# Optimization experiments

Measured on AMD Instinct MI355X. Metric: run time of the kernel, lower is better.

## Reference

```python
import jax, jax.numpy as jnp
import numpy as np
from jax import lax

B, N, C = 16, 16384, 256          # batch, points, seed feature dim
P, NS = 256, 16                   # num_proposal, ball-query nsample
RADIUS = 0.3
NUM_CLASS, NUM_HEADING_BIN, NUM_SIZE = 18, 12, 18
OUT_FEAT = 2 + 3 + NUM_HEADING_BIN * 2 + NUM_SIZE * 4 + NUM_CLASS   # 119
PN2_NC = 128
MID_FEAT = (PN2_NC + OUT_FEAT) // 2                                 # 123
EPS = 1e-5

PARAM_NAMES = [f"mlp_{s}{i}" for i in range(3) for s in ("w", "b", "g", "be")] + [
    "c1_w", "c1_b", "bn1_g", "bn1_b", "c2_w", "c2_b", "bn2_g", "bn2_b", "c3_w", "c3_b"]


def setup_inputs():
    key = jax.random.key(0)
    ks = iter(jax.random.split(key, 32))
    def w(shape):
        return jax.random.normal(next(ks), shape, jnp.float32) / np.float32(np.sqrt(shape[0]))
    inp = {
        "pos":      jax.random.normal(next(ks), (B, N, 3), jnp.float32),
        "features": jax.random.normal(next(ks), (B, C, N), jnp.float32),
        "seed_pos": jax.random.normal(next(ks), (B, N, 3), jnp.float32),
    }
    dims = [3 + C, PN2_NC, PN2_NC, PN2_NC]
    for i in range(3):
        inp[f"mlp_w{i}"]  = w((dims[i], dims[i + 1]))
        inp[f"mlp_b{i}"]  = jnp.zeros((dims[i + 1],), jnp.float32)
        inp[f"mlp_g{i}"]  = jnp.ones((dims[i + 1],), jnp.float32)
        inp[f"mlp_be{i}"] = jnp.zeros((dims[i + 1],), jnp.float32)
    inp["c1_w"], inp["c1_b"] = w((PN2_NC, PN2_NC)), jnp.zeros((PN2_NC,), jnp.float32)
    inp["bn1_g"], inp["bn1_b"] = jnp.ones((PN2_NC,), jnp.float32), jnp.zeros((PN2_NC,), jnp.float32)
    inp["c2_w"], inp["c2_b"] = w((PN2_NC, MID_FEAT)), jnp.zeros((MID_FEAT,), jnp.float32)
    inp["bn2_g"], inp["bn2_b"] = jnp.ones((MID_FEAT,), jnp.float32), jnp.zeros((MID_FEAT,), jnp.float32)
    inp["c3_w"], inp["c3_b"] = w((MID_FEAT, OUT_FEAT)), jnp.zeros((OUT_FEAT,), jnp.float32)
    return inp


def _fps(p):
    # iterative furthest point sampling on one cloud p:[N,3] -> [P] int32 (starts at index 0)
    def step(carry, _):
        dists, far = carry
        d = jnp.sum((p - p[far]) ** 2, axis=-1)
        dists = jnp.minimum(dists, d)
        return (dists, jnp.argmax(dists).astype(jnp.int32)), far
    init = (jnp.full((p.shape[0],), 1e10, p.dtype), jnp.array(0, jnp.int32))
    _, idx = lax.scan(step, init, None, length=P)
    return idx


def _ball_query(new_pos, pos):
    # first NS points of pos within RADIUS of each center (CUDA ball_query semantics)
    d2 = jnp.sum((new_pos[:, :, None, :] - pos[:, None, :, :]) ** 2, -1)  # [B,P,N]
    n = pos.shape[1]
    ar = jnp.arange(n, dtype=jnp.int32)
    sortkey = jnp.where(d2 <= RADIUS ** 2, ar, ar + n)
    vals, idx = lax.top_k(-sortkey, NS)        # smallest keys = earliest in-radius indices
    valid = (-vals) < n
    return jnp.where(valid, idx, idx[..., :1])  # pad misses with first hit


def _bn(x, g, b, axes):
    m = jnp.mean(x, axes, keepdims=True)
    v = jnp.var(x, axes, keepdims=True)
    return (x - m) * lax.rsqrt(v + EPS) * g + b


def _forward(pos, features, seed_pos, params):
    idx_p = jax.vmap(_fps)(seed_pos)                              # seed_fps sampling [B,P]
    take = jax.vmap(lambda a, i: a[i])
    new_pos = take(pos, idx_p)                                    # [B,P,3]
    idx = _ball_query(new_pos, pos)                               # [B,P,NS]
    gp = take(pos, idx.reshape(B, -1)).reshape(B, P, NS, 3)
    gf = take(features.transpose(0, 2, 1), idx.reshape(B, -1)).reshape(B, P, NS, C)
    x = jnp.concatenate([gp - new_pos[:, :, None, :], gf], -1)    # [B,P,NS,3+C]
    for i in range(3):                                            # shared MLP (1x1 conv2d + BN + ReLU)
        x = jax.nn.relu(_bn(x @ params[f"mlp_w{i}"] + params[f"mlp_b{i}"],
                            params[f"mlp_g{i}"], params[f"mlp_be{i}"], (0, 1, 2)))
    x = jnp.max(x, axis=2)                                        # max over neighbors -> [B,P,128]
    x = jax.nn.relu(_bn(x @ params["c1_w"] + params["c1_b"], params["bn1_g"], params["bn1_b"], (0, 1)))
    x = jax.nn.relu(_bn(x @ params["c2_w"] + params["c2_b"], params["bn2_g"], params["bn2_b"], (0, 1)))
    x = x @ params["c3_w"] + params["c3_b"]                       # [B,P,OUT_FEAT]
    return x.transpose(0, 2, 1)                                   # [B,OUT_FEAT,P] like torch Conv1d


def reference(pos, features, seed_pos, mlp_w0, mlp_b0, mlp_g0, mlp_be0, mlp_w1, mlp_b1, mlp_g1, mlp_be1, mlp_w2, mlp_b2, mlp_g2, mlp_be2, c1_w, c1_b, bn1_g, bn1_b, c2_w, c2_b, bn2_g, bn2_b, c3_w, c3_b):
    ps = [mlp_w0, mlp_b0, mlp_g0, mlp_be0, mlp_w1, mlp_b1, mlp_g1, mlp_be1,
          mlp_w2, mlp_b2, mlp_g2, mlp_be2, c1_w, c1_b, bn1_g, bn1_b,
          c2_w, c2_b, bn2_g, bn2_b, c3_w, c3_b]
    params = dict(zip(PARAM_NAMES, ps))
    return _forward(pos, features, seed_pos, params)
```

## Files before the change

### kernel.cpp

```cpp
#include <hip/hip_runtime.h>

#define N_PTS 16384
#define BATCH 16
#define NPROP 256
#define NSAMP 16
#define CFEAT 256
#define KIN 259
#define KPAD 264
#define MBIG 65536
#define MSMALL 4096
#define NOUT 119

#define FPS_LIST(M) M(0) M(1) M(2) M(3) M(4) M(5) M(6) M(7) \
  M(8) M(9) M(10) M(11) M(12) M(13) M(14) M(15) \
  M(16) M(17) M(18) M(19) M(20) M(21) M(22) M(23) \
  M(24) M(25) M(26) M(27) M(28) M(29) M(30) M(31)

#define FPS_PIN8(a,b,c,d,e,f,g,h) \
  asm volatile("" : "+v"(a), "+v"(b), "+v"(c), "+v"(d), \
                    "+v"(e), "+v"(f), "+v"(g), "+v"(h));

__global__ __attribute__((amdgpu_flat_work_group_size(512,512), amdgpu_waves_per_eu(2,2)))
void fps_kernel(const float* __restrict__ sp, int* __restrict__ idx_p) {
#pragma clang fp contract(off)
  const int b = blockIdx.x;
  const int t = threadIdx.x;
  const int w = t >> 6;
  const int lane = t & 63;
  const float* base = sp + (size_t)b * N_PTS * 3;

#define FPS_DECL(J) float px##J, py##J, pz##J, dd##J;
  FPS_LIST(FPS_DECL)
#undef FPS_DECL

#define FPS_INIT(J) { const int i = t + J*512; \
    px##J = base[i*3+0]; py##J = base[i*3+1]; pz##J = base[i*3+2]; \
    dd##J = 1e10f; }
  FPS_LIST(FPS_INIT)
#undef FPS_INIT

  FPS_PIN8(px0,px1,px2,px3,px4,px5,px6,px7)
  FPS_PIN8(px8,px9,px10,px11,px12,px13,px14,px15)
  FPS_PIN8(px16,px17,px18,px19,px20,px21,px22,px23)
  FPS_PIN8(px24,px25,px26,px27,px28,px29,px30,px31)
  FPS_PIN8(py0,py1,py2,py3,py4,py5,py6,py7)
  FPS_PIN8(py8,py9,py10,py11,py12,py13,py14,py15)
  FPS_PIN8(py16,py17,py18,py19,py20,py21,py22,py23)
  FPS_PIN8(py24,py25,py26,py27,py28,py29,py30,py31)
  FPS_PIN8(pz0,pz1,pz2,pz3,pz4,pz5,pz6,pz7)
  FPS_PIN8(pz8,pz9,pz10,pz11,pz12,pz13,pz14,pz15)
  FPS_PIN8(pz16,pz17,pz18,pz19,pz20,pz21,pz22,pz23)
  FPS_PIN8(pz24,pz25,pz26,pz27,pz28,pz29,pz30,pz31)

  if (t == 0) idx_p[b*NPROP] = 0;
  float fx = base[0], fy = base[1], fz = base[2];
  __shared__ unsigned long long part[2][8];
  for (int it = 1; it < NPROP; ++it) {
    float mv = -1.0f; int mi = 0;
#define FPS_STEP(J) { \
    float dx = px##J - fx, dy = py##J - fy, dz = pz##J - fz; \
    float d = (dx*dx + dy*dy) + dz*dz; \
    float nd = fminf(dd##J, d); \
    dd##J = nd; \
    if (nd > mv) { mv = nd; mi = t + J*512; } }
    FPS_LIST(FPS_STEP)
#undef FPS_STEP
    unsigned long long key =
      ((unsigned long long)__float_as_uint(mv) << 32) |
      (unsigned long long)(unsigned)(0x7FFFFFFF - mi);
#pragma unroll
    for (int o = 32; o > 0; o >>= 1) {
      unsigned long long ok = __shfl_xor(key, o, 64);
      if (ok > key) key = ok;
    }
    const int buf = it & 1;
    if (lane == 0) part[buf][w] = key;
    __syncthreads();
    unsigned long long k2 = part[buf][0];
#pragma unroll
    for (int q = 1; q < 8; ++q) {
      unsigned long long ok = part[buf][q];
      if (ok > k2) k2 = ok;
    }
    const int far = 0x7FFFFFFF - (int)(unsigned)(k2 & 0xFFFFFFFFull);
    if (t == 0) idx_p[b*NPROP + it] = far;
    const float* fp = base + (size_t)far*3;
    fx = fp[0]; fy = fp[1]; fz = fp[2];
  }
}

__global__ __launch_bounds__(256)
void newpos_kernel(const float* __restrict__ pos, const int* __restrict__ idx_p,
                   float* __restrict__ npos) {
  int g = blockIdx.x*256 + threadIdx.x;
  if (g >= BATCH*NPROP) return;
  int b = g >> 8;
  int ii = idx_p[g];
  const float* pp = pos + ((size_t)b*N_PTS + ii)*3;
  npos[g*3+0] = pp[0]; npos[g*3+1] = pp[1]; npos[g*3+2] = pp[2];
}

__global__ __launch_bounds__(256)
void ballq_kernel(const float* __restrict__ pos, const float* __restrict__ npos,
                  int* __restrict__ idxg) {
#pragma clang fp contract(off)
  __shared__ int res[4][NSAMP];
  const int tid = threadIdx.x;
  const int w = tid >> 6, lane = tid & 63;
  const int cid = blockIdx.x*4 + w;
  const int b = cid >> 8;
  const float R2 = (float)(0.3*0.3);
  if (lane == 0) res[w][0] = 0;
  const float cx = npos[cid*3+0], cy = npos[cid*3+1], cz = npos[cid*3+2];
  const float* pb = pos + (size_t)b*N_PTS*3;
  int cnt = 0;
  const unsigned long long lmask = (1ull << lane) - 1ull;
#pragma unroll 4
  for (int ch = 0; ch < N_PTS/64; ++ch) {
    int i = ch*64 + lane;
    float dx = pb[i*3+0]-cx, dy = pb[i*3+1]-cy, dz = pb[i*3+2]-cz;
    float d2 = (dx*dx + dy*dy) + dz*dz;
    bool pred = d2 <= R2;
    unsigned long long bal = __ballot(pred);
    if (pred) {
      int slot = cnt + (int)__popcll(bal & lmask);
      if (slot < NSAMP) res[w][slot] = i;
    }
    cnt += (int)__popcll(bal);
  }
  __syncthreads();
  if (lane < NSAMP) {
    int v = res[w][lane];
    if (lane >= cnt) v = res[w][0];
    idxg[cid*NSAMP + lane] = v;
  }
}

__global__ __launch_bounds__(256)
void prep_w(const float* __restrict__ w0, const float* __restrict__ c2w,
            const float* __restrict__ c2b, const float* __restrict__ c3w,
            const float* __restrict__ c3b,
            float* __restrict__ Wp0, float* __restrict__ Wp2, float* __restrict__ B2p,
            float* __restrict__ Wp3, float* __restrict__ B3p) {
  int g = blockIdx.x*256 + threadIdx.x;
  const int S0 = KPAD*128, S1 = S0 + 16384, S2 = S1 + 128, S3 = S2 + 16384, S4 = S3 + 128;
  if (g < S0) {
    int k = g >> 7, n = g & 127;
    Wp0[g] = (k < KIN) ? w0[k*128 + n] : 0.f;
  } else if (g < S1) {
    int g2 = g - S0; int k = g2 >> 7, n = g2 & 127;
    Wp2[g2] = (n < 123) ? c2w[k*123 + n] : 0.f;
  } else if (g < S2) {
    int n = g - S1;
    B2p[n] = (n < 123) ? c2b[n] : 0.f;
  } else if (g < S3) {
    int g2 = g - S2; int k = g2 >> 7, n = g2 & 127;
    Wp3[g2] = (k < 123 && n < NOUT) ? c3w[k*NOUT + n] : 0.f;
  } else if (g < S4) {
    int n = g - S3;
    B3p[n] = (n < NOUT) ? c3b[n] : 0.f;
  }
}

__global__ __launch_bounds__(256)
void gemm_l0(const float* __restrict__ pos, const float* __restrict__ npos,
             const float* __restrict__ feat, const int* __restrict__ idxg,
             const float* __restrict__ Wp, const float* __restrict__ bias,
             float* __restrict__ H) {
  __shared__ float As[8][128];
  __shared__ float Ws[8][128];
  __shared__ float pd[3][128];
  __shared__ int ids[128];
  const int tid = threadIdx.x;
  const int m0 = blockIdx.x * 128;
  const int b = m0 >> 12;
  const float* fb = feat + (size_t)b * CFEAT * N_PTS;
  if (tid < 128) {
    int m = m0 + tid;
    int ii = idxg[m];
    ids[tid] = ii;
    int q = m >> 4;
    const float* pp = pos + ((size_t)b*N_PTS + ii)*3;
    const float* cc = npos + (size_t)q*3;
    pd[0][tid] = pp[0] - cc[0];
    pd[1][tid] = pp[1] - cc[1];
    pd[2][tid] = pp[2] - cc[2];
  }
  __syncthreads();
  const int kr = tid >> 5;
  const int cm = (tid & 31) * 4;
  int ii_r[4];
#pragma unroll
  for (int x = 0; x < 4; ++x) ii_r[x] = ids[cm+x];
  float acc[8][8];
#pragma unroll
  for (int i = 0; i < 8; ++i)
#pragma unroll
    for (int j = 0; j < 8; ++j) acc[i][j] = 0.f;
  const int tm = tid & 15, tn = tid >> 4;
  for (int k0 = 0; k0 < KPAD; k0 += 8) {
    const int k = k0 + kr;
    float4 a0;
    if (k < 3) {
      a0.x = pd[k][cm+0]; a0.y = pd[k][cm+1]; a0.z = pd[k][cm+2]; a0.w = pd[k][cm+3];
    } else if (k < KIN) {
      const float* fr = fb + (size_t)(k-3)*N_PTS;
      a0.x = fr[ii_r[0]]; a0.y = fr[ii_r[1]]; a0.z = fr[ii_r[2]]; a0.w = fr[ii_r[3]];
    } else {
      a0 = make_float4(0.f,0.f,0.f,0.f);
    }
    float4 wv = *(const float4*)(Wp + (size_t)k*128 + cm);
    __syncthreads();
    *(float4*)&As[kr][cm] = a0;
    *(float4*)&Ws[kr][cm] = wv;
    __syncthreads();
#pragma unroll
    for (int kk = 0; kk < 8; ++kk) {
      float a[8], bb[8];
      *(float4*)(a)   = *(const float4*)&As[kk][tm*4];
      *(float4*)(a+4) = *(const float4*)&As[kk][tm*4 + 64];
      *(float4*)(bb)   = *(const float4*)&Ws[kk][tn*8];
      *(float4*)(bb+4) = *(const float4*)&Ws[kk][tn*8+4];
#pragma unroll
      for (int i = 0; i < 8; ++i)
#pragma unroll
        for (int j = 0; j < 8; ++j)
          acc[i][j] = fmaf(a[i], bb[j], acc[i][j]);
    }
  }
#pragma unroll
  for (int j = 0; j < 8; ++j) {
    const int n = tn*8 + j;
    const float bv = bias[n];
    float* cr = H + (size_t)n*MBIG + m0 + tm*4;
    float4 o0, o1;
    o0.x = acc[0][j]+bv; o0.y = acc[1][j]+bv; o0.z = acc[2][j]+bv; o0.w = acc[3][j]+bv;
    o1.x = acc[4][j]+bv; o1.y = acc[5][j]+bv; o1.z = acc[6][j]+bv; o1.w = acc[7][j]+bv;
    *(float4*)(cr)      = o0;
    *(float4*)(cr + 64) = o1;
  }
}

template<int TM, int MODE>
__global__ __launch_bounds__(256)
void gemm_k(const float* __restrict__ A, const float* __restrict__ W,
            const float* __restrict__ bias, const float* __restrict__ sc,
            const float* __restrict__ sh, float* __restrict__ C,
            int M, int K, int useT) {
  __shared__ float As[8][TM];
  __shared__ float Ws[8][128];
  const int tid = threadIdx.x;
  const int m0 = blockIdx.x * TM;
  const int kr = tid >> 5;
  const int cw = (tid & 31) * 4;
  const int tm = tid & 15, tn = tid >> 4;
  constexpr int MR = TM / 16;
  float acc[MR][8];
#pragma unroll
  for (int i = 0; i < MR; ++i)
#pragma unroll
    for (int j = 0; j < 8; ++j) acc[i][j] = 0.f;
  for (int k0 = 0; k0 < K; k0 += 8) {
    const float* ar = A + (size_t)(k0+kr)*M + m0;
    float4 wv = *(const float4*)(W + (size_t)(k0+kr)*128 + cw);
    const float s_ = useT ? sc[k0+kr] : 1.f;
    const float h_ = useT ? sh[k0+kr] : 0.f;
    if constexpr (TM == 128) {
      float4 a0 = *(const float4*)(ar + cw);
      if (useT) {
        a0.x = fmaxf(fmaf(a0.x, s_, h_), 0.f);
        a0.y = fmaxf(fmaf(a0.y, s_, h_), 0.f);
        a0.z = fmaxf(fmaf(a0.z, s_, h_), 0.f);
        a0.w = fmaxf(fmaf(a0.w, s_, h_), 0.f);
      }
      __syncthreads();
      *(float4*)&As[kr][cw] = a0;
      *(float4*)&Ws[kr][cw] = wv;
      __syncthreads();
    } else {
      const int c2 = (tid & 31) * 2;
      float2 a0 = *(const float2*)(ar + c2);
      if (useT) {
        a0.x = fmaxf(fmaf(a0.x, s_, h_), 0.f);
        a0.y = fmaxf(fmaf(a0.y, s_, h_), 0.f);
      }
      __syncthreads();
      *(float2*)&As[kr][c2] = a0;
      *(float4*)&Ws[kr][cw] = wv;
      __syncthreads();
    }
#pragma unroll
    for (int kk = 0; kk < 8; ++kk) {
      float a[MR], bb[8];
      *(float4*)(a) = *(const float4*)&As[kk][tm*4];
      if constexpr (MR == 8)
        *(float4*)(a+4) = *(const float4*)&As[kk][tm*4 + 64];
      *(float4*)(bb)   = *(const float4*)&Ws[kk][tn*8];
      *(float4*)(bb+4) = *(const float4*)&Ws[kk][tn*8+4];
#pragma unroll
      for (int i = 0; i < MR; ++i)
#pragma unroll
        for (int j = 0; j < 8; ++j)
          acc[i][j] = fmaf(a[i], bb[j], acc[i][j]);
    }
  }
  if (MODE == 0) {
#pragma unroll
    for (int j = 0; j < 8; ++j) {
      const int n = tn*8 + j;
      const float bv = bias[n];
      float* cr = C + (size_t)n*M + m0 + tm*4;
      float4 o0;
      o0.x = acc[0][j]+bv; o0.y = acc[1][j]+bv; o0.z = acc[2][j]+bv; o0.w = acc[3][j]+bv;
      *(float4*)(cr) = o0;
      if constexpr (MR == 8) {
        float4 o1;
        o1.x = acc[4][j]+bv; o1.y = acc[5][j]+bv; o1.z = acc[6][j]+bv; o1.w = acc[7][j]+bv;
        *(float4*)(cr + 64) = o1;
      }
    }
  } else {
    const int bb_ = m0 >> 8;
    const int pcol = (m0 & 255) + tm*4;
#pragma unroll
    for (int j = 0; j < 8; ++j) {
      const int n = tn*8 + j;
      if (n < NOUT) {
        const float bv = bias[n];
        float* cr = C + ((size_t)bb_*NOUT + n)*256 + pcol;
        float4 o0;
        o0.x = acc[0][j]+bv; o0.y = acc[1][j]+bv; o0.z = acc[2][j]+bv; o0.w = acc[3][j]+bv;
        *(float4*)(cr) = o0;
      }
    }
  }
}

__global__ __launch_bounds__(1024)
void stats_kernel(const float* __restrict__ H, int M, int nc,
                  const float* __restrict__ g, const float* __restrict__ be,
                  float* __restrict__ sc, float* __restrict__ sh) {
  const int c = blockIdx.x;
  const int tid = threadIdx.x;
  if (c >= nc) { if (tid == 0) { sc[c] = 0.f; sh[c] = 0.f; } return; }
  const float* row = H + (size_t)c * M;
  float s = 0.f, q = 0.f;
  for (int i = tid*4; i < M; i += 4096) {
    float4 v = *(const float4*)(row + i);
    s += v.x + v.y + v.z + v.w;
    q += v.x*v.x + v.y*v.y + v.z*v.z + v.w*v.w;
  }
#pragma unroll
  for (int o = 32; o > 0; o >>= 1) {
    s += __shfl_xor(s, o, 64);
    q += __shfl_xor(q, o, 64);
  }
  __shared__ float ws_[16], wq_[16];
  const int w = tid >> 6, lane = tid & 63;
  if (lane == 0) { ws_[w] = s; wq_[w] = q; }
  __syncthreads();
  if (tid == 0) {
    float S = 0.f, Q = 0.f;
#pragma unroll
    for (int k = 0; k < 16; ++k) { S += ws_[k]; Q += wq_[k]; }
    float mean = S / (float)M;
    float var  = Q / (float)M - mean*mean;
    float inv  = rsqrtf(var + 1e-5f);
    float gg = g[c];
    sc[c] = inv * gg;
    sh[c] = be[c] - mean * inv * gg;
  }
}

__global__ __launch_bounds__(256)
void pool_kernel(const float* __restrict__ H2, const float* __restrict__ sc,
                 const float* __restrict__ sh, float* __restrict__ X3) {
  int gidx = blockIdx.x*256 + threadIdx.x;
  int c = gidx >> 12;
  int q = gidx & 4095;
  const float* src = H2 + (size_t)c*MBIG + (size_t)q*NSAMP;
  float s_ = sc[c], h_ = sh[c];
  float m = 0.f;
#pragma unroll
  for (int k = 0; k < NSAMP; k += 4) {
    float4 v = *(const float4*)(src + k);
    m = fmaxf(m, fmaf(v.x, s_, h_));
    m = fmaxf(m, fmaf(v.y, s_, h_));
    m = fmaxf(m, fmaf(v.z, s_, h_));
    m = fmaxf(m, fmaf(v.w, s_, h_));
  }
  X3[(size_t)c*MSMALL + q] = m;
}

extern "C" void kernel_launch(void* const* d_in, const int* in_sizes, int n_in,
                              void* d_out, int out_size, void* d_ws, size_t ws_size,
                              hipStream_t stream) {
  const float* pos  = (const float*)d_in[0];
  const float* feat = (const float*)d_in[1];
  const float* spos = (const float*)d_in[2];
  const float* w0  = (const float*)d_in[3];
  const float* b0  = (const float*)d_in[4];
  const float* g0  = (const float*)d_in[5];
  const float* be0 = (const float*)d_in[6];
  const float* w1  = (const float*)d_in[7];
  const float* b1  = (const float*)d_in[8];
  const float* g1  = (const float*)d_in[9];
  const float* be1 = (const float*)d_in[10];
  const float* w2  = (const float*)d_in[11];
  const float* b2  = (const float*)d_in[12];
  const float* g2  = (const float*)d_in[13];
  const float* be2 = (const float*)d_in[14];
  const float* c1w = (const float*)d_in[15];
  const float* c1b = (const float*)d_in[16];
  const float* bg1 = (const float*)d_in[17];
  const float* bb1 = (const float*)d_in[18];
  const float* c2w = (const float*)d_in[19];
  const float* c2b = (const float*)d_in[20];
  const float* bg2 = (const float*)d_in[21];
  const float* bb2 = (const float*)d_in[22];
  const float* c3w = (const float*)d_in[23];
  const float* c3b = (const float*)d_in[24];
  float* out = (float*)d_out;

  float* fws = (float*)d_ws;
  float* H0  = fws;
  float* H1  = H0 + (size_t)128*MBIG;
  float* X3  = H1 + (size_t)128*MBIG;
  float* H3  = X3 + (size_t)128*MSMALL;
  float* H4  = H3 + (size_t)128*MSMALL;
  float* Wp0 = H4 + (size_t)128*MSMALL;
  float* Wp2 = Wp0 + KPAD*128;
  float* B2p = Wp2 + 16384;
  float* Wp3 = B2p + 128;
  float* B3p = Wp3 + 16384;
  float* sc0 = B3p + 128; float* sh0 = sc0 + 128;
  float* sc1 = sh0 + 128; float* sh1 = sc1 + 128;
  float* sc2 = sh1 + 128; float* sh2 = sc2 + 128;
  float* sc3 = sh2 + 128; float* sh3 = sc3 + 128;
  float* sc4 = sh3 + 128; float* sh4 = sc4 + 128;
  float* npos = sh4 + 128;
  int* idx_p = (int*)(npos + (size_t)BATCH*NPROP*3);
  int* idxg  = idx_p + BATCH*NPROP;
  float* H2 = H0;

  fps_kernel<<<BATCH, 512, 0, stream>>>(spos, idx_p);
  newpos_kernel<<<16, 256, 0, stream>>>(pos, idx_p, npos);
  ballq_kernel<<<BATCH*NPROP/4, 256, 0, stream>>>(pos, npos, idxg);
  prep_w<<<261, 256, 0, stream>>>(w0, c2w, c2b, c3w, c3b, Wp0, Wp2, B2p, Wp3, B3p);

  gemm_l0<<<MBIG/128, 256, 0, stream>>>(pos, npos, feat, idxg, Wp0, b0, H0);
  stats_kernel<<<128, 1024, 0, stream>>>(H0, MBIG, 128, g0, be0, sc0, sh0);
  gemm_k<128,0><<<MBIG/128, 256, 0, stream>>>(H0, w1, b1, sc0, sh0, H1, MBIG, 128, 1);
  stats_kernel<<<128, 1024, 0, stream>>>(H1, MBIG, 128, g1, be1, sc1, sh1);
  gemm_k<128,0><<<MBIG/128, 256, 0, stream>>>(H1, w2, b2, sc1, sh1, H2, MBIG, 128, 1);
  stats_kernel<<<128, 1024, 0, stream>>>(H2, MBIG, 128, g2, be2, sc2, sh2);
  pool_kernel<<<128*MSMALL/256, 256, 0, stream>>>(H2, sc2, sh2, X3);

  gemm_k<64,0><<<MSMALL/64, 256, 0, stream>>>(X3, c1w, c1b, nullptr, nullptr, H3, MSMALL, 128, 0);
  stats_kernel<<<128, 1024, 0, stream>>>(H3, MSMALL, 128, bg1, bb1, sc3, sh3);
  gemm_k<64,0><<<MSMALL/64, 256, 0, stream>>>(H3, Wp2, B2p, sc3, sh3, H4, MSMALL, 128, 1);
  stats_kernel<<<128, 1024, 0, stream>>>(H4, MSMALL, 123, bg2, bb2, sc4, sh4);
  gemm_k<64,1><<<MSMALL/64, 256, 0, stream>>>(H4, Wp3, B3p, sc4, sh4, out, MSMALL, 128, 1);
}
```

Measured before the change: 871.1 us.

## Split layer-0 gather into separate kernel writing packed row-major input

Adds a gather kernel that writes the grouped features and relative positions into a padded row-major workspace buffer, then a plain GEMM kernel that reads contiguous rows instead of doing indirect gathers inside the GEMM loop. The aim is to take the scattered feature loads out of the compute-bound GEMM. In exchange it adds a 65536x264 float round trip through global memory and one extra launch. The new path runs only when the workspace is large enough, otherwise the old fused kernel is used.

Result: slower. 1.012 ms (+16.2%).

```diff
diff --git a/kernel.cpp b/kernel.cpp
--- a/kernel.cpp
+++ b/kernel.cpp
@@ -159,6 +159,87 @@
   } else if (g < S4) {
     int n = g - S3;
     B3p[n] = (n < NOUT) ? c3b[n] : 0.f;
+  }
+}
+
+__global__ __launch_bounds__(256)
+void gather_kernel(const float* __restrict__ feat, const float* __restrict__ pos,
+                   const float* __restrict__ npos, const int* __restrict__ idxg,
+                   float* __restrict__ Xg) {
+#pragma clang fp contract(off)
+  const int b  = blockIdx.x >> 4;
+  const int ct = blockIdx.x & 15;
+  const int tid = threadIdx.x;
+  const float* fb = feat + ((size_t)b * CFEAT + (size_t)ct*16) * N_PTS;
+  for (int s = 0; s < 16; ++s) {
+    const int mb = s*256 + tid;
+    const int m  = b*4096 + mb;
+    const int ii = idxg[m];
+    float* dst = Xg + (size_t)m*KPAD + 3 + ct*16;
+#pragma unroll
+    for (int c = 0; c < 16; ++c)
+      dst[c] = fb[(size_t)c*N_PTS + ii];
+    if (ct == 0) {
+      const float* pp = pos + ((size_t)b*N_PTS + ii)*3;
+      const float* cc = npos + (size_t)(m >> 4)*3;
+      float* d0 = Xg + (size_t)m*KPAD;
+      d0[0] = pp[0]-cc[0]; d0[1] = pp[1]-cc[1]; d0[2] = pp[2]-cc[2];
+      d0[259] = 0.f; d0[260] = 0.f; d0[261] = 0.f; d0[262] = 0.f; d0[263] = 0.f;
+    }
+  }
+}
+
+__global__ __launch_bounds__(256)
+void gemm_l0v2(const float* __restrict__ Xg, const float* __restrict__ Wp,
+               const float* __restrict__ bias, float* __restrict__ H) {
+  __shared__ float As[8][132];
+  __shared__ float Ws[8][128];
+  const int tid = threadIdx.x;
+  const int m0 = blockIdx.x * 128;
+  const int mL = tid & 127, half = tid >> 7;
+  const int kr = tid >> 5;
+  const int cw = (tid & 31) * 4;
+  const int tm = tid & 15, tn = tid >> 4;
+  const float* myrow = Xg + (size_t)(m0 + mL)*KPAD + half*4;
+  float acc[8][8];
+#pragma unroll
+  for (int i = 0; i < 8; ++i)
+#pragma unroll
+    for (int j = 0; j < 8; ++j) acc[i][j] = 0.f;
+  for (int k0 = 0; k0 < KPAD; k0 += 8) {
+    float4 av = *(const float4*)(myrow + k0);
+    float4 wv = *(const float4*)(Wp + (size_t)(k0+kr)*128 + cw);
+    __syncthreads();
+    As[half*4+0][mL] = av.x;
+    As[half*4+1][mL] = av.y;
+    As[half*4+2][mL] = av.z;
+    As[half*4+3][mL] = av.w;
+    *(float4*)&Ws[kr][cw] = wv;
+    __syncthreads();
+#pragma unroll
+    for (int kk = 0; kk < 8; ++kk) {
+      float a[8], bb[8];
+      *(float4*)(a)   = *(const float4*)&As[kk][tm*4];
+      *(float4*)(a+4) = *(const float4*)&As[kk][tm*4 + 64];
+      *(float4*)(bb)   = *(const float4*)&Ws[kk][tn*8];
+      *(float4*)(bb+4) = *(const float4*)&Ws[kk][tn*8+4];
+#pragma unroll
+      for (int i = 0; i < 8; ++i)
+#pragma unroll
+        for (int j = 0; j < 8; ++j)
+          acc[i][j] = fmaf(a[i], bb[j], acc[i][j]);
+    }
+  }
+#pragma unroll
+  for (int j = 0; j < 8; ++j) {
+    const int n = tn*8 + j;
+    const float bv = bias[n];
+    float* cr = H + (size_t)n*MBIG + m0 + tm*4;
+    float4 o0, o1;
+    o0.x = acc[0][j]+bv; o0.y = acc[1][j]+bv; o0.z = acc[2][j]+bv; o0.w = acc[3][j]+bv;
+    o1.x = acc[4][j]+bv; o1.y = acc[5][j]+bv; o1.z = acc[6][j]+bv; o1.w = acc[7][j]+bv;
+    *(float4*)(cr)      = o0;
+    *(float4*)(cr + 64) = o1;
   }
 }
 
@@ -423,24 +504,28 @@
   float* out = (float*)d_out;
 
   float* fws = (float*)d_ws;
-  float* H0  = fws;
-  float* H1  = H0 + (size_t)128*MBIG;
-  float* X3  = H1 + (size_t)128*MBIG;
-  float* H3  = X3 + (size_t)128*MSMALL;
-  float* H4  = H3 + (size_t)128*MSMALL;
-  float* Wp0 = H4 + (size_t)128*MSMALL;
-  float* Wp2 = Wp0 + KPAD*128;
-  float* B2p = Wp2 + 16384;
-  float* Wp3 = B2p + 128;
-  float* B3p = Wp3 + 16384;
-  float* sc0 = B3p + 128; float* sh0 = sc0 + 128;
-  float* sc1 = sh0 + 128; float* sh1 = sc1 + 128;
-  float* sc2 = sh1 + 128; float* sh2 = sc2 + 128;
-  float* sc3 = sh2 + 128; float* sh3 = sc3 + 128;
-  float* sc4 = sh3 + 128; float* sh4 = sc4 + 128;
-  float* npos = sh4 + 128;
-  int* idx_p = (int*)(npos + (size_t)BATCH*NPROP*3);
-  int* idxg  = idx_p + BATCH*NPROP;
+  size_t off = 0;
+  auto alloc = [&](size_t n) { float* p = fws + off; off += n; return p; };
+  float* H0  = alloc((size_t)128*MBIG);
+  float* H1  = alloc((size_t)128*MBIG);
+  float* X3  = alloc((size_t)128*MSMALL);
+  float* H3  = alloc((size_t)128*MSMALL);
+  float* H4  = alloc((size_t)128*MSMALL);
+  float* Wp0 = alloc(KPAD*128);
+  float* Wp2 = alloc(16384);
+  float* B2p = alloc(128);
+  float* Wp3 = alloc(16384);
+  float* B3p = alloc(128);
+  float* sc0 = alloc(128); float* sh0 = alloc(128);
+  float* sc1 = alloc(128); float* sh1 = alloc(128);
+  float* sc2 = alloc(128); float* sh2 = alloc(128);
+  float* sc3 = alloc(128); float* sh3 = alloc(128);
+  float* sc4 = alloc(128); float* sh4 = alloc(128);
+  float* npos = alloc((size_t)BATCH*NPROP*3);
+  int* idx_p = (int*)alloc(BATCH*NPROP);
+  int* idxg  = (int*)alloc(MBIG);
+  float* Xg  = alloc((size_t)MBIG*KPAD);
+  const bool bigws = ws_size >= off * sizeof(float);
   float* H2 = H0;
 
   fps_kernel<<<BATCH, 512, 0, stream>>>(spos, idx_p);
@@ -448,7 +533,12 @@
   ballq_kernel<<<BATCH*NPROP/4, 256, 0, stream>>>(pos, npos, idxg);
   prep_w<<<261, 256, 0, stream>>>(w0, c2w, c2b, c3w, c3b, Wp0, Wp2, B2p, Wp3, B3p);
 
-  gemm_l0<<<MBIG/128, 256, 0, stream>>>(pos, npos, feat, idxg, Wp0, b0, H0);
+  if (bigws) {
+    gather_kernel<<<BATCH*16, 256, 0, stream>>>(feat, pos, npos, idxg, Xg);
+    gemm_l0v2<<<MBIG/128, 256, 0, stream>>>(Xg, Wp0, b0, H0);
+  } else {
+    gemm_l0<<<MBIG/128, 256, 0, stream>>>(pos, npos, feat, idxg, Wp0, b0, H0);
+  }
   stats_kernel<<<128, 1024, 0, stream>>>(H0, MBIG, 128, g0, be0, sc0, sh0);
   gemm_k<128,0><<<MBIG/128, 256, 0, stream>>>(H0, w1, b1, sc0, sh0, H1, MBIG, 128, 1);
   stats_kernel<<<128, 1024, 0, stream>>>(H1, MBIG, 128, g1, be1, sc1, sh1);
```

## Fuse BN statistics partial sums into GEMM epilogues and newpos into FPS

Applied to the files above, without the earlier changes.

Each GEMM epilogue now reduces per-block channel sums and sums of squares with wave shuffles and writes them to a partial buffer. A small finish kernel then turns those partials into BN scale and shift, so the separate full rereads of the 32 MB activation tensors are gone. The newpos gather is folded into the end of the FPS kernel through a shared index list, which removes one launch. In exchange the epilogues do extra shuffle work and writes, and the summation order changes, which can shift results slightly.

Result: no change. 860.6 us (-1.2%).

```diff
diff --git a/kernel.cpp b/kernel.cpp
--- a/kernel.cpp
+++ b/kernel.cpp
@@ -10,6 +10,8 @@
 #define MBIG 65536
 #define MSMALL 4096
 #define NOUT 119
+#define NBLK_BIG 512
+#define NBLK_SMALL 64
 
 #define FPS_LIST(M) M(0) M(1) M(2) M(3) M(4) M(5) M(6) M(7) \
   M(8) M(9) M(10) M(11) M(12) M(13) M(14) M(15) \
@@ -21,7 +23,8 @@
                     "+v"(e), "+v"(f), "+v"(g), "+v"(h));
 
 __global__ __attribute__((amdgpu_flat_work_group_size(512,512), amdgpu_waves_per_eu(2,2)))
-void fps_kernel(const float* __restrict__ sp, int* __restrict__ idx_p) {
+void fps_kernel(const float* __restrict__ sp, const float* __restrict__ pos,
+                int* __restrict__ idx_p, float* __restrict__ npos) {
 #pragma clang fp contract(off)
   const int b = blockIdx.x;
   const int t = threadIdx.x;
@@ -52,9 +55,10 @@
   FPS_PIN8(pz16,pz17,pz18,pz19,pz20,pz21,pz22,pz23)
   FPS_PIN8(pz24,pz25,pz26,pz27,pz28,pz29,pz30,pz31)
 
-  if (t == 0) idx_p[b*NPROP] = 0;
+  __shared__ unsigned long long part[2][8];
+  __shared__ int sidx[NPROP];
+  if (t == 0) { idx_p[b*NPROP] = 0; sidx[0] = 0; }
   float fx = base[0], fy = base[1], fz = base[2];
-  __shared__ unsigned long long part[2][8];
   for (int it = 1; it < NPROP; ++it) {
     float mv = -1.0f; int mi = 0;
 #define FPS_STEP(J) { \
@@ -83,21 +87,17 @@
       if (ok > k2) k2 = ok;
     }
     const int far = 0x7FFFFFFF - (int)(unsigned)(k2 & 0xFFFFFFFFull);
-    if (t == 0) idx_p[b*NPROP + it] = far;
+    if (t == 0) { idx_p[b*NPROP + it] = far; sidx[it] = far; }
     const float* fp = base + (size_t)far*3;
     fx = fp[0]; fy = fp[1]; fz = fp[2];
   }
-}
-
-__global__ __launch_bounds__(256)
-void newpos_kernel(const float* __restrict__ pos, const int* __restrict__ idx_p,
-                   float* __restrict__ npos) {
-  int g = blockIdx.x*256 + threadIdx.x;
-  if (g >= BATCH*NPROP) return;
-  int b = g >> 8;
-  int ii = idx_p[g];
-  const float* pp = pos + ((size_t)b*N_PTS + ii)*3;
-  npos[g*3+0] = pp[0]; npos[g*3+1] = pp[1]; npos[g*3+2] = pp[2];
+  __syncthreads();
+  if (t < NPROP) {
+    const int ii = sidx[t];
+    const float* pp = pos + ((size_t)b*N_PTS + ii)*3;
+    float* np = npos + (size_t)(b*NPROP + t)*3;
+    np[0] = pp[0]; np[1] = pp[1]; np[2] = pp[2];
+  }
 }
 
 __global__ __launch_bounds__(256)
@@ -166,7 +166,7 @@
 void gemm_l0(const float* __restrict__ pos, const float* __restrict__ npos,
              const float* __restrict__ feat, const int* __restrict__ idxg,
              const float* __restrict__ Wp, const float* __restrict__ bias,
-             float* __restrict__ H) {
+             float* __restrict__ H, float* __restrict__ Sp, float* __restrict__ Qp) {
   __shared__ float As[8][128];
   __shared__ float Ws[8][128];
   __shared__ float pd[3][128];
@@ -238,14 +238,27 @@
     o1.x = acc[4][j]+bv; o1.y = acc[5][j]+bv; o1.z = acc[6][j]+bv; o1.w = acc[7][j]+bv;
     *(float4*)(cr)      = o0;
     *(float4*)(cr + 64) = o1;
-  }
-}
-
-template<int TM, int MODE>
+    float s = o0.x+o0.y+o0.z+o0.w + o1.x+o1.y+o1.z+o1.w;
+    float q = o0.x*o0.x+o0.y*o0.y+o0.z*o0.z+o0.w*o0.w
+            + o1.x*o1.x+o1.y*o1.y+o1.z*o1.z+o1.w*o1.w;
+#pragma unroll
+    for (int o = 1; o < 16; o <<= 1) {
+      s += __shfl_xor(s, o, 64);
+      q += __shfl_xor(q, o, 64);
+    }
+    if (tm == 0) {
+      Sp[(size_t)n*NBLK_BIG + blockIdx.x] = s;
+      Qp[(size_t)n*NBLK_BIG + blockIdx.x] = q;
+    }
+  }
+}
+
+template<int TM, int MODE, int DOPART>
 __global__ __launch_bounds__(256)
 void gemm_k(const float* __restrict__ A, const float* __restrict__ W,
             const float* __restrict__ bias, const float* __restrict__ sc,
             const float* __restrict__ sh, float* __restrict__ C,
+            float* __restrict__ Sp, float* __restrict__ Qp,
             int M, int K, int useT) {
   __shared__ float As[8][TM];
   __shared__ float Ws[8][128];
@@ -255,6 +268,7 @@
   const int cw = (tid & 31) * 4;
   const int tm = tid & 15, tn = tid >> 4;
   constexpr int MR = TM / 16;
+  constexpr int NBLK = (TM == 128) ? NBLK_BIG : NBLK_SMALL;
   float acc[MR][8];
 #pragma unroll
   for (int i = 0; i < MR; ++i)
@@ -310,13 +324,29 @@
       const int n = tn*8 + j;
       const float bv = bias[n];
       float* cr = C + (size_t)n*M + m0 + tm*4;
-      float4 o0;
+      float4 o0, o1;
       o0.x = acc[0][j]+bv; o0.y = acc[1][j]+bv; o0.z = acc[2][j]+bv; o0.w = acc[3][j]+bv;
       *(float4*)(cr) = o0;
       if constexpr (MR == 8) {
-        float4 o1;
         o1.x = acc[4][j]+bv; o1.y = acc[5][j]+bv; o1.z = acc[6][j]+bv; o1.w = acc[7][j]+bv;
         *(float4*)(cr + 64) = o1;
+      }
+      if constexpr (DOPART) {
+        float s = o0.x+o0.y+o0.z+o0.w;
+        float q = o0.x*o0.x+o0.y*o0.y+o0.z*o0.z+o0.w*o0.w;
+        if constexpr (MR == 8) {
+          s += o1.x+o1.y+o1.z+o1.w;
+          q += o1.x*o1.x+o1.y*o1.y+o1.z*o1.z+o1.w*o1.w;
+        }
+#pragma unroll
+        for (int o = 1; o < 16; o <<= 1) {
+          s += __shfl_xor(s, o, 64);
+          q += __shfl_xor(q, o, 64);
+        }
+        if (tm == 0) {
+          Sp[(size_t)n*NBLK + blockIdx.x] = s;
+          Qp[(size_t)n*NBLK + blockIdx.x] = q;
+        }
       }
     }
   } else {
@@ -336,33 +366,31 @@
   }
 }
 
-__global__ __launch_bounds__(1024)
-void stats_kernel(const float* __restrict__ H, int M, int nc,
+__global__ __launch_bounds__(256)
+void stats_finish(const float* __restrict__ Sp, const float* __restrict__ Qp,
+                  int nblk, int M, int nc,
                   const float* __restrict__ g, const float* __restrict__ be,
                   float* __restrict__ sc, float* __restrict__ sh) {
   const int c = blockIdx.x;
   const int tid = threadIdx.x;
   if (c >= nc) { if (tid == 0) { sc[c] = 0.f; sh[c] = 0.f; } return; }
-  const float* row = H + (size_t)c * M;
   float s = 0.f, q = 0.f;
-  for (int i = tid*4; i < M; i += 4096) {
-    float4 v = *(const float4*)(row + i);
-    s += v.x + v.y + v.z + v.w;
-    q += v.x*v.x + v.y*v.y + v.z*v.z + v.w*v.w;
+  for (int i = tid; i < nblk; i += 256) {
+    s += Sp[(size_t)c*nblk + i];
+    q += Qp[(size_t)c*nblk + i];
   }
 #pragma unroll
   for (int o = 32; o > 0; o >>= 1) {
     s += __shfl_xor(s, o, 64);
     q += __shfl_xor(q, o, 64);
   }
-  __shared__ float ws_[16], wq_[16];
+  __shared__ float ws_[4], wq_[4];
   const int w = tid >> 6, lane = tid & 63;
   if (lane == 0) { ws_[w] = s; wq_[w] = q; }
   __syncthreads();
   if (tid == 0) {
-    float S = 0.f, Q = 0.f;
-#pragma unroll
-    for (int k = 0; k < 16; ++k) { S += ws_[k]; Q += wq_[k]; }
+    float S = ws_[0]+ws_[1]+ws_[2]+ws_[3];
+    float Q = wq_[0]+wq_[1]+wq_[2]+wq_[3];
     float mean = S / (float)M;
     float var  = Q / (float)M - mean*mean;
     float inv  = rsqrtf(var + 1e-5f);
@@ -423,42 +451,45 @@
   float* out = (float*)d_out;
 
   float* fws = (float*)d_ws;
-  float* H0  = fws;
-  float* H1  = H0 + (size_t)128*MBIG;
-  float* X3  = H1 + (size_t)128*MBIG;
-  float* H3  = X3 + (size_t)128*MSMALL;
-  float* H4  = H3 + (size_t)128*MSMALL;
-  float* Wp0 = H4 + (size_t)128*MSMALL;
-  float* Wp2 = Wp0 + KPAD*128;
-  float* B2p = Wp2 + 16384;
-  float* Wp3 = B2p + 128;
-  float* B3p = Wp3 + 16384;
-  float* sc0 = B3p + 128; float* sh0 = sc0 + 128;
-  float* sc1 = sh0 + 128; float* sh1 = sc1 + 128;
-  float* sc2 = sh1 + 128; float* sh2 = sc2 + 128;
-  float* sc3 = sh2 + 128; float* sh3 = sc3 + 128;
-  float* sc4 = sh3 + 128; float* sh4 = sc4 + 128;
-  float* npos = sh4 + 128;
-  int* idx_p = (int*)(npos + (size_t)BATCH*NPROP*3);
-  int* idxg  = idx_p + BATCH*NPROP;
+  size_t off = 0;
+  auto alloc = [&](size_t n) { float* p = fws + off; off += n; return p; };
+  float* H0  = alloc((size_t)128*MBIG);
+  float* H1  = alloc((size_t)128*MBIG);
+  float* X3  = alloc((size_t)128*MSMALL);
+  float* H3  = alloc((size_t)128*MSMALL);
+  float* H4  = alloc((size_t)128*MSMALL);
+  float* Wp0 = alloc(KPAD*128);
+  float* Wp2 = alloc(16384);
+  float* B2p = alloc(128);
+  float* Wp3 = alloc(16384);
+  float* B3p = alloc(128);
+  float* sc0 = alloc(128); float* sh0 = alloc(128);
+  float* sc1 = alloc(128); float* sh1 = alloc(128);
+  float* sc2 = alloc(128); float* sh2 = alloc(128);
+  float* sc3 = alloc(128); float* sh3 = alloc(128);
+  float* sc4 = alloc(128); float* sh4 = alloc(128);
+  float* Sp  = alloc((size_t)128*NBLK_BIG);
+  float* Qp  = alloc((size_t)128*NBLK_BIG);
+  float* npos = alloc((size_t)BATCH*NPROP*3);
+  int* idx_p = (int*)alloc(BATCH*NPROP);
+  int* idxg  = (int*)alloc(MBIG);
   float* H2 = H0;
 
-  fps_kernel<<<BATCH, 512, 0, stream>>>(spos, idx_p);
-  newpos_kernel<<<16, 256, 0, stream>>>(pos, idx_p, npos);
+  fps_kernel<<<BATCH, 512, 0, stream>>>(spos, pos, idx_p, npos);
   ballq_kernel<<<BATCH*NPROP/4, 256, 0, stream>>>(pos, npos, idxg);
   prep_w<<<261, 256, 0, stream>>>(w0, c2w, c2b, c3w, c3b, Wp0, Wp2, B2p, Wp3, B3p);
 
-  gemm_l0<<<MBIG/128, 256, 0, stream>>>(pos, npos, feat, idxg, Wp0, b0, H0);
-  stats_kernel<<<128, 1024, 0, stream>>>(H0, MBIG, 128, g0, be0, sc0, sh0);
-  gemm_k<128,0><<<MBIG/128, 256, 0, stream>>>(H0, w1, b1, sc0, sh0, H1, MBIG, 128, 1);
-  stats_kernel<<<128, 1024, 0, stream>>>(H1, MBIG, 128, g1, be1, sc1, sh1);
-  gemm_k<128,0><<<MBIG/128, 256, 0, stream>>>(H1, w2, b2, sc1, sh1, H2, MBIG, 128, 1);
-  stats_kernel<<<128, 1024, 0, stream>>>(H2, MBIG, 128, g2, be2, sc2, sh2);
+  gemm_l0<<<MBIG/128, 256, 0, stream>>>(pos, npos, feat, idxg, Wp0, b0, H0, Sp, Qp);
+  stats_finish<<<128, 256, 0, stream>>>(Sp, Qp, NBLK_BIG, MBIG, 128, g0, be0, sc0, sh0);
+  gemm_k<128,0,1><<<MBIG/128, 256, 0, stream>>>(H0, w1, b1, sc0, sh0, H1, Sp, Qp, MBIG, 128, 1);
+  stats_finish<<<128, 256, 0, stream>>>(Sp, Qp, NBLK_BIG, MBIG, 128, g1, be1, sc1, sh1);
+  gemm_k<128,0,1><<<MBIG/128, 256, 0, stream>>>(H1, w2, b2, sc1, sh1, H2, Sp, Qp, MBIG, 128, 1);
+  stats_finish<<<128, 256, 0, stream>>>(Sp, Qp, NBLK_BIG, MBIG, 128, g2, be2, sc2, sh2);
   pool_kernel<<<128*MSMALL/256, 256, 0, stream>>>(H2, sc2, sh2, X3);
 
-  gemm_k<64,0><<<MSMALL/64, 256, 0, stream>>>(X3, c1w, c1b, nullptr, nullptr, H3, MSMALL, 128, 0);
-  stats_kernel<<<128, 1024, 0, stream>>>(H3, MSMALL, 128, bg1, bb1, sc3, sh3);
-  gemm_k<64,0><<<MSMALL/64, 256, 0, stream>>>(H3, Wp2, B2p, sc3, sh3, H4, MSMALL, 128, 1);
-  stats_kernel<<<128, 1024, 0, stream>>>(H4, MSMALL, 123, bg2, bb2, sc4, sh4);
-  gemm_k<64,1><<<MSMALL/64, 256, 0, stream>>>(H4, Wp3, B3p, sc4, sh4, out, MSMALL, 128, 1);
-}
+  gemm_k<64,0,1><<<MSMALL/64, 256, 0, stream>>>(X3, c1w, c1b, nullptr, nullptr, H3, Sp, Qp, MSMALL, 128, 0);
+  stats_finish<<<128, 256, 0, stream>>>(Sp, Qp, NBLK_SMALL, MSMALL, 128, bg1, bb1, sc3, sh3);
+  gemm_k<64,0,1><<<MSMALL/64, 256, 0, stream>>>(H3, Wp2, B2p, sc3, sh3, H4, Sp, Qp, MSMALL, 128, 1);
+  stats_finish<<<128, 256, 0, stream>>>(Sp, Qp, NBLK_SMALL, MSMALL, 123, bg2, bb2, sc4, sh4);
+  gemm_k<64,1,0><<<MSMALL/64, 256, 0, stream>>>(H4, Wp3, B3p, sc4, sh4, out, nullptr, nullptr, MSMALL, 128, 1);
+}
```
